# Performance work log

Hardware: AMD Instinct MI355X
Metric: run time of the kernel (lower is better)

The kernel has to match this reference:

```python
import jax, jax.numpy as jnp
import numpy as np

NUM_ENT = 30000
NUM_ATTR_VALUES = 10000
NUM_NODES = NUM_ENT + NUM_ATTR_VALUES
NUM_REL = 230
NUM_ATTR_TYPES = 10
HIDDEN = 200          # num_bases=200 -> 1x1 block decomposition (per-rel diagonal)
N_EDGES = 600000
TIME_INTERVAL = 24
NUM_TIMESTAMPS = 365
PERIOD = 7
TRANX = 0.1
AMPY = 0.005
BATCH = 4096
RRELU_SLOPE = (1.0 / 8.0 + 1.0 / 3.0) / 2.0  # F.rrelu in eval mode


def setup_inputs() -> dict:
    key = jax.random.key(0)
    ks = jax.random.split(key, 12)
    ent_emb = jax.random.normal(ks[0], (NUM_ENT, HIDDEN), jnp.float32)            # nn.init.normal_
    attr_emb = jax.random.normal(ks[1], (NUM_ATTR_VALUES, HIDDEN), jnp.float32) * 0.05
    rel_emb = jax.random.normal(ks[2], (NUM_REL, HIDDEN), jnp.float32) * 0.1
    t = jnp.arange(NUM_TIMESTAMPS, dtype=jnp.float32)
    time_emb = (AMPY * (jnp.sin(2.0 * jnp.pi * t / PERIOD) + 1.0) + TRANX)[:, None]  # (T,1), frozen
    # RGCNBlockLayer weight: (num_rels, num_bases*submat_in*submat_out) = (10, 200)
    rgcn_weight = jax.random.normal(ks[3], (NUM_ATTR_TYPES, HIDDEN), jnp.float32) * 0.1
    dec_W = jax.random.normal(ks[4], (HIDDEN, 2 * HIDDEN + 1), jnp.float32) * 0.05
    dec_b = jnp.zeros((HIDDEN,), jnp.float32)
    edge_src = jax.random.randint(ks[5], (N_EDGES,), 0, NUM_NODES)
    edge_dst = jax.random.randint(ks[6], (N_EDGES,), 0, NUM_NODES)
    edge_type = jax.random.randint(ks[7], (N_EDGES,), 0, NUM_ATTR_TYPES)
    deg = jax.ops.segment_sum(jnp.ones((N_EDGES,), jnp.float32), edge_dst, num_segments=NUM_NODES)
    norm = (1.0 / jnp.clip(deg, 1.0))[:, None]  # (NUM_NODES, 1) in-degree norm
    ent_idx = jax.random.randint(ks[8], (BATCH,), 0, NUM_ENT)
    rel_idx = jax.random.randint(ks[9], (BATCH,), 0, NUM_REL)
    obj_idx = jax.random.randint(ks[10], (BATCH,), 0, NUM_ENT)
    time_raw = jax.random.randint(ks[11], (BATCH,), 0, NUM_TIMESTAMPS * TIME_INTERVAL)
    batch_data = jnp.stack([ent_idx, rel_idx, obj_idx, time_raw], axis=1)  # (B, 4)
    return {
        'ent_emb': ent_emb, 'attr_emb': attr_emb, 'rel_emb': rel_emb,
        'time_emb': time_emb, 'rgcn_weight': rgcn_weight,
        'dec_W': dec_W, 'dec_b': dec_b, 'norm': norm,
        'edge_src': edge_src, 'edge_dst': edge_dst, 'edge_type': edge_type,
        'batch_data': batch_data,
    }


def reference(ent_emb, attr_emb, rel_emb, time_emb, rgcn_weight, dec_W, dec_b,
              norm, edge_src, edge_dst, edge_type, batch_data):
    # --- RGCNBlockLayer (1x1 blocks): gather, per-relation diagonal multiply, scatter-sum ---
    h0 = jnp.concatenate([ent_emb, attr_emb], axis=0)           # (N, H)
    msg = h0[edge_src] * rgcn_weight[edge_type]                  # (E, H)
    agg = jax.ops.segment_sum(msg, edge_dst, num_segments=h0.shape[0])
    h = agg * norm                                               # apply_func: h * norm
    h = jnp.where(h >= 0, h, RRELU_SLOPE * h)                    # rrelu (eval); dropout=identity
    static_emb = h[:NUM_ENT]                                     # (num_ent, H)
    # --- embedding lookups ---
    ent = static_emb[batch_data[:, 0]]                           # (B, H)
    rel = rel_emb[batch_data[:, 1]]                              # (B, H)
    tim = time_emb[batch_data[:, 3] // TIME_INTERVAL]            # (B, 1)
    # --- decoder: tanh -> cat -> linear -> (dropout) -> relu -> mm ---
    x = jnp.concatenate([jnp.tanh(ent), rel, tim], axis=1)       # (B, 2H+1)
    x = x @ dec_W.T + dec_b                                      # (B, H)
    x = jax.nn.relu(x)
    return x @ static_emb.T                                      # (B, num_ent)
```

## Files before the change

### kernel.cpp

```cpp
#include <hip/hip_runtime.h>
#include <hip/hip_bf16.h>

#define NUM_ENT   30000
#define NUM_ATTR  10000
#define NUM_NODES 40000
#define NUM_TYPES 10
#define HIDDEN    200
#define KPAD      224
#define XP        416
#define NPAD      30080
#define N_EDGES   600000
#define BATCH     4096
#define XDIM      401
#define RRELU_SLOPE 0.22916666666666666f

using bf16x8 = __attribute__((ext_vector_type(8))) short;
using f32x4  = __attribute__((ext_vector_type(4))) float;
typedef __hip_bfloat16 bf16;

__device__ inline float bf2f(ushort u) { return __uint_as_float((unsigned)u << 16); }

__global__ void k_cvt(const float* __restrict__ ent, const float* __restrict__ attr,
                      ushort* __restrict__ h0b) {
    int i4 = blockIdx.x * blockDim.x + threadIdx.x;
    if (i4 >= NUM_NODES * HIDDEN / 4) return;
    int base = i4 * 4;
    const float* src = (base < NUM_ENT * HIDDEN) ? ent + base
                                                 : attr + (base - NUM_ENT * HIDDEN);
    float4 v = *reinterpret_cast<const float4*>(src);
    ushort4 o;
    o.x = __bfloat16_as_ushort(__float2bfloat16(v.x));
    o.y = __bfloat16_as_ushort(__float2bfloat16(v.y));
    o.z = __bfloat16_as_ushort(__float2bfloat16(v.z));
    o.w = __bfloat16_as_ushort(__float2bfloat16(v.w));
    *reinterpret_cast<ushort4*>(h0b + base) = o;
}

__global__ __launch_bounds__(1024) void k_prep(const float* __restrict__ norm,
                                               int* __restrict__ offsets,
                                               int* __restrict__ cursor) {
    __shared__ int part[1024];
    int t = threadIdx.x;
    const int CH = (NUM_ENT + 1023) / 1024;
    int base = t * CH;
    int caps[CH];
    int s = 0;
    for (int i = 0; i < CH; ++i) {
        int idx = base + i;
        int c = 0;
        if (idx < NUM_ENT) c = (int)(1.0f / norm[idx] + 0.5f);
        caps[i] = c;
        s += c;
    }
    part[t] = s;
    __syncthreads();
    for (int off = 1; off < 1024; off <<= 1) {
        int v = (t >= off) ? part[t - off] : 0;
        __syncthreads();
        part[t] += v;
        __syncthreads();
    }
    int run = (t == 0) ? 0 : part[t - 1];
    for (int i = 0; i < CH; ++i) {
        int idx = base + i;
        if (idx < NUM_ENT) {
            offsets[idx] = run;
            cursor[idx]  = run;
            run += caps[i];
        }
    }
}

__global__ void k_place(const int* __restrict__ edst, const int* __restrict__ esrc,
                        const int* __restrict__ etype, int* __restrict__ cursor,
                        int* __restrict__ sorted) {
    int e = blockIdx.x * blockDim.x + threadIdx.x;
    if (e < N_EDGES) {
        int d = edst[e];
        if (d < NUM_ENT) {
            int p = atomicAdd(&cursor[d], 1);
            sorted[p] = (esrc[e] << 4) | etype[e];
        }
    }
}

__global__ void k_aggregate(const ushort* __restrict__ h0b, const float* __restrict__ w,
                            const int* __restrict__ offsets, const int* __restrict__ cursor,
                            const int* __restrict__ sorted, const float* __restrict__ norm,
                            bf16* __restrict__ S) {
    __shared__ float wl[NUM_TYPES * HIDDEN];
    for (int i = threadIdx.x; i < NUM_TYPES * HIDDEN; i += blockDim.x)
        wl[i] = w[i];
    __syncthreads();

    int n    = (blockIdx.x * blockDim.x + threadIdx.x) >> 6;
    int lane = threadIdx.x & 63;
    if (n >= NPAD) return;

    if (n >= NUM_ENT) {
        if (lane < KPAD / 4) {
            bf16 z4[4] = {};
            *reinterpret_cast<uint2*>(S + (size_t)n * KPAD + lane * 4) =
                *reinterpret_cast<uint2*>(z4);
        }
        return;
    }

    int beg = offsets[n], end = cursor[n];
    bool act = lane < 50;
    int  c   = lane * 4;

    float4 a0 = make_float4(0, 0, 0, 0), a1 = a0, a2 = a0, a3 = a0;
    int e = beg;
    for (; e + 4 <= end; e += 4) {
        int r0 = sorted[e + 0], r1 = sorted[e + 1], r2 = sorted[e + 2], r3 = sorted[e + 3];
        if (act) {
            ushort4 h0 = *reinterpret_cast<const ushort4*>(h0b + (size_t)(r0 >> 4) * HIDDEN + c);
            ushort4 h1 = *reinterpret_cast<const ushort4*>(h0b + (size_t)(r1 >> 4) * HIDDEN + c);
            ushort4 h2 = *reinterpret_cast<const ushort4*>(h0b + (size_t)(r2 >> 4) * HIDDEN + c);
            ushort4 h3 = *reinterpret_cast<const ushort4*>(h0b + (size_t)(r3 >> 4) * HIDDEN + c);
            const float* w0 = &wl[(r0 & 15) * HIDDEN + c];
            const float* w1 = &wl[(r1 & 15) * HIDDEN + c];
            const float* w2 = &wl[(r2 & 15) * HIDDEN + c];
            const float* w3 = &wl[(r3 & 15) * HIDDEN + c];
            a0.x += bf2f(h0.x) * w0[0]; a0.y += bf2f(h0.y) * w0[1];
            a0.z += bf2f(h0.z) * w0[2]; a0.w += bf2f(h0.w) * w0[3];
            a1.x += bf2f(h1.x) * w1[0]; a1.y += bf2f(h1.y) * w1[1];
            a1.z += bf2f(h1.z) * w1[2]; a1.w += bf2f(h1.w) * w1[3];
            a2.x += bf2f(h2.x) * w2[0]; a2.y += bf2f(h2.y) * w2[1];
            a2.z += bf2f(h2.z) * w2[2]; a2.w += bf2f(h2.w) * w2[3];
            a3.x += bf2f(h3.x) * w3[0]; a3.y += bf2f(h3.y) * w3[1];
            a3.z += bf2f(h3.z) * w3[2]; a3.w += bf2f(h3.w) * w3[3];
        }
    }
    for (; e < end; ++e) {
        int r0 = sorted[e];
        if (act) {
            ushort4 h0 = *reinterpret_cast<const ushort4*>(h0b + (size_t)(r0 >> 4) * HIDDEN + c);
            const float* w0 = &wl[(r0 & 15) * HIDDEN + c];
            a0.x += bf2f(h0.x) * w0[0]; a0.y += bf2f(h0.y) * w0[1];
            a0.z += bf2f(h0.z) * w0[2]; a0.w += bf2f(h0.w) * w0[3];
        }
    }

    if (act) {
        float nm = norm[n];
        float v0 = (a0.x + a1.x + a2.x + a3.x) * nm;
        float v1 = (a0.y + a1.y + a2.y + a3.y) * nm;
        float v2 = (a0.z + a1.z + a2.z + a3.z) * nm;
        float v3 = (a0.w + a1.w + a2.w + a3.w) * nm;
        v0 = (v0 >= 0.f) ? v0 : RRELU_SLOPE * v0;
        v1 = (v1 >= 0.f) ? v1 : RRELU_SLOPE * v1;
        v2 = (v2 >= 0.f) ? v2 : RRELU_SLOPE * v2;
        v3 = (v3 >= 0.f) ? v3 : RRELU_SLOPE * v3;
        bf16 t4[4] = {__float2bfloat16(v0), __float2bfloat16(v1),
                      __float2bfloat16(v2), __float2bfloat16(v3)};
        *reinterpret_cast<uint2*>(S + (size_t)n * KPAD + lane * 4) =
            *reinterpret_cast<uint2*>(t4);
    } else if (lane < KPAD / 4) {
        bf16 z4[4] = {};
        *reinterpret_cast<uint2*>(S + (size_t)n * KPAD + lane * 4) =
            *reinterpret_cast<uint2*>(z4);
    }
}

__global__ void k_build_XW(const bf16* __restrict__ S, const float* __restrict__ rel_emb,
                           const float* __restrict__ time_emb, const float* __restrict__ dec_W,
                           const int* __restrict__ batch, bf16* __restrict__ X,
                           bf16* __restrict__ Wb) {
    int b = blockIdx.x;
    if (b < BATCH) {
        int m = b;
        int e  = batch[m * 4 + 0];
        int rl = batch[m * 4 + 1];
        int tr = batch[m * 4 + 3];
        float tv = time_emb[tr / 24];
        for (int c = threadIdx.x; c < XP; c += 256) {
            float v;
            if (c < HIDDEN) {
                v = tanhf(__bfloat162float(S[(size_t)e * KPAD + c]));
            } else if (c < 2 * HIDDEN) {
                v = rel_emb[(size_t)rl * HIDDEN + (c - HIDDEN)];
            } else if (c == 2 * HIDDEN) {
                v = tv;
            } else {
                v = 0.f;
            }
            X[(size_t)m * XP + c] = __float2bfloat16(v);
        }
    } else {
        int n = b - BATCH;
        for (int c = threadIdx.x; c < XP; c += 256) {
            float v = (n < HIDDEN && c < XDIM) ? dec_W[(size_t)n * XDIM + c] : 0.f;
            Wb[(size_t)n * XP + c] = __float2bfloat16(v);
        }
    }
}

__global__ __launch_bounds__(256) void k_dec_gemm(const bf16* __restrict__ Xb,
                                                  const bf16* __restrict__ Wbb,
                                                  const float* __restrict__ dec_b,
                                                  bf16* __restrict__ Y) {
    int wid  = threadIdx.x >> 6;
    int lane = threadIdx.x & 63;
    int row0 = blockIdx.x * 64 + wid * 16;
    int rsel = lane & 15;
    int koff = (lane >> 4) * 8;

    const short* Xp = reinterpret_cast<const short*>(Xb);
    const short* Wp = reinterpret_cast<const short*>(Wbb);

    f32x4 acc[14] = {};
#pragma unroll
    for (int kt = 0; kt < 13; ++kt) {
        int kbase = kt * 32 + koff;
        bf16x8 a = *reinterpret_cast<const bf16x8*>(Xp + (size_t)(row0 + rsel) * XP + kbase);
#pragma unroll
        for (int j = 0; j < 14; ++j) {
            bf16x8 b = *reinterpret_cast<const bf16x8*>(Wp + (size_t)(j * 16 + rsel) * XP + kbase);
            acc[j] = __builtin_amdgcn_mfma_f32_16x16x32_bf16(a, b, acc[j], 0, 0, 0);
        }
    }

    int crow = (lane >> 4) * 4;
    int ccol = lane & 15;
#pragma unroll
    for (int j = 0; j < 14; ++j) {
        int col = j * 16 + ccol;
        float bias = (col < HIDDEN) ? dec_b[col] : 0.f;
#pragma unroll
        for (int r = 0; r < 4; ++r) {
            int row = row0 + crow + r;
            float v = fmaxf(acc[j][r] + bias, 0.f);
            Y[(size_t)row * KPAD + col] = __float2bfloat16(v);
        }
    }
}

__global__ __launch_bounds__(256) void k_gemm(const bf16* __restrict__ Yb,
                                              const bf16* __restrict__ Sb,
                                              float* __restrict__ out) {
    int bid = blockIdx.x;
    int xcd = bid & 7;
    int t   = (bid >> 3) + xcd * 940;
    int ytile = t & 31;
    int xtile = t >> 5;

    int wid  = threadIdx.x >> 6;
    int lane = threadIdx.x & 63;
    int wm = wid >> 1, wn = wid & 1;
    int row0 = ytile * 128 + wm * 64;
    int col0 = xtile * 128 + wn * 64;
    int rsel = lane & 15;
    int koff = (lane >> 4) * 8;

    const short* Yp = reinterpret_cast<const short*>(Yb);
    const short* Sp = reinterpret_cast<const short*>(Sb);

    f32x4 acc[4][4] = {};
#pragma unroll
    for (int kt = 0; kt < 7; ++kt) {
        int kbase = kt * 32 + koff;
        bf16x8 a[4], b[4];
#pragma unroll
        for (int i = 0; i < 4; ++i)
            a[i] = *reinterpret_cast<const bf16x8*>(Yp + (size_t)(row0 + i * 16 + rsel) * KPAD + kbase);
#pragma unroll
        for (int j = 0; j < 4; ++j)
            b[j] = *reinterpret_cast<const bf16x8*>(Sp + (size_t)(col0 + j * 16 + rsel) * KPAD + kbase);
#pragma unroll
        for (int i = 0; i < 4; ++i)
#pragma unroll
            for (int j = 0; j < 4; ++j)
                acc[i][j] = __builtin_amdgcn_mfma_f32_16x16x32_bf16(a[i], b[j], acc[i][j], 0, 0, 0);
    }

    int crow = (lane >> 4) * 4;
    int ccol = lane & 15;
#pragma unroll
    for (int i = 0; i < 4; ++i)
#pragma unroll
        for (int j = 0; j < 4; ++j) {
            int col = col0 + j * 16 + ccol;
            if (col >= NUM_ENT) continue;
#pragma unroll
            for (int r = 0; r < 4; ++r) {
                int row = row0 + i * 16 + crow + r;
                out[(size_t)row * NUM_ENT + col] = acc[i][j][r];
            }
        }
}

extern "C" void kernel_launch(void* const* d_in, const int* in_sizes, int n_in,
                              void* d_out, int out_size, void* d_ws, size_t ws_size,
                              hipStream_t stream) {
    const float* ent_emb  = (const float*)d_in[0];
    const float* attr_emb = (const float*)d_in[1];
    const float* rel_emb  = (const float*)d_in[2];
    const float* time_emb = (const float*)d_in[3];
    const float* rgcn_w   = (const float*)d_in[4];
    const float* dec_W    = (const float*)d_in[5];
    const float* dec_b    = (const float*)d_in[6];
    const float* norm     = (const float*)d_in[7];
    const int*   esrc     = (const int*)d_in[8];
    const int*   edst     = (const int*)d_in[9];
    const int*   etype    = (const int*)d_in[10];
    const int*   batch    = (const int*)d_in[11];

    char* ws = (char*)d_ws;
    bf16*   S      = (bf16*)ws;
    bf16*   Y      = (bf16*)(ws + 13475840);
    int*    offs   = (int*)(ws + 15310848);
    int*    cursor = (int*)(ws + 15430912);
    int*    sorted = (int*)(ws + 15550976);
    bf16*   X      = (bf16*)(ws + 18070976);
    bf16*   Wb     = (bf16*)(ws + 21478848);
    ushort* h0b    = (ushort*)(ws + 21665216);

    k_cvt  <<<(NUM_NODES * HIDDEN / 4 + 255) / 256, 256, 0, stream>>>(ent_emb, attr_emb, h0b);
    k_prep <<<1, 1024, 0, stream>>>(norm, offs, cursor);
    k_place<<<(N_EDGES + 255) / 256, 256, 0, stream>>>(edst, esrc, etype, cursor, sorted);
    k_aggregate<<<NPAD * 64 / 256, 256, 0, stream>>>(h0b, rgcn_w, offs, cursor, sorted, norm, S);
    k_build_XW<<<BATCH + KPAD, 256, 0, stream>>>(S, rel_emb, time_emb, dec_W, batch, X, Wb);
    k_dec_gemm<<<BATCH / 64, 256, 0, stream>>>(X, Wb, dec_b, Y);
    k_gemm<<<7520, 256, 0, stream>>>(Y, S, (float*)d_out);
}
```

Baseline: 395.2 us.

## Split node aggregation across two waves and stage GEMM output through LDS

```diff
diff --git a/kernel.cpp b/kernel.cpp
--- a/kernel.cpp
+++ b/kernel.cpp
@@ -89,78 +89,93 @@
                             const int* __restrict__ sorted, const float* __restrict__ norm,
                             bf16* __restrict__ S) {
     __shared__ float wl[NUM_TYPES * HIDDEN];
+    __shared__ float part[2][200];
     for (int i = threadIdx.x; i < NUM_TYPES * HIDDEN; i += blockDim.x)
         wl[i] = w[i];
     __syncthreads();
 
-    int n    = (blockIdx.x * blockDim.x + threadIdx.x) >> 6;
+    int wid  = threadIdx.x >> 6;
     int lane = threadIdx.x & 63;
-    if (n >= NPAD) return;
-
-    if (n >= NUM_ENT) {
-        if (lane < KPAD / 4) {
+    int ln   = wid >> 1;
+    int sub  = wid & 1;
+    int n    = blockIdx.x * 2 + ln;
+    bool live = (n < NUM_ENT);
+    bool act  = lane < 50;
+    int  c    = lane * 4;
+
+    float4 a0 = make_float4(0, 0, 0, 0), a1 = a0, a2 = a0, a3 = a0;
+    if (live) {
+        int beg = offsets[n], end = cursor[n];
+        int mid = beg + ((end - beg + 1) >> 1);
+        int lo = sub ? mid : beg;
+        int hi = sub ? end : mid;
+        int e = lo;
+        for (; e + 4 <= hi; e += 4) {
+            int r0 = sorted[e + 0], r1 = sorted[e + 1], r2 = sorted[e + 2], r3 = sorted[e + 3];
+            if (act) {
+                ushort4 h0 = *reinterpret_cast<const ushort4*>(h0b + (size_t)(r0 >> 4) * HIDDEN + c);
+                ushort4 h1 = *reinterpret_cast<const ushort4*>(h0b + (size_t)(r1 >> 4) * HIDDEN + c);
+                ushort4 h2 = *reinterpret_cast<const ushort4*>(h0b + (size_t)(r2 >> 4) * HIDDEN + c);
+                ushort4 h3 = *reinterpret_cast<const ushort4*>(h0b + (size_t)(r3 >> 4) * HIDDEN + c);
+                const float* w0 = &wl[(r0 & 15) * HIDDEN + c];
+                const float* w1 = &wl[(r1 & 15) * HIDDEN + c];
+                const float* w2 = &wl[(r2 & 15) * HIDDEN + c];
+                const float* w3 = &wl[(r3 & 15) * HIDDEN + c];
+                a0.x += bf2f(h0.x) * w0[0]; a0.y += bf2f(h0.y) * w0[1];
+                a0.z += bf2f(h0.z) * w0[2]; a0.w += bf2f(h0.w) * w0[3];
+                a1.x += bf2f(h1.x) * w1[0]; a1.y += bf2f(h1.y) * w1[1];
+                a1.z += bf2f(h1.z) * w1[2]; a1.w += bf2f(h1.w) * w1[3];
+                a2.x += bf2f(h2.x) * w2[0]; a2.y += bf2f(h2.y) * w2[1];
+                a2.z += bf2f(h2.z) * w2[2]; a2.w += bf2f(h2.w) * w2[3];
+                a3.x += bf2f(h3.x) * w3[0]; a3.y += bf2f(h3.y) * w3[1];
+                a3.z += bf2f(h3.z) * w3[2]; a3.w += bf2f(h3.w) * w3[3];
+            }
+        }
+        for (; e < hi; ++e) {
+            int r0 = sorted[e];
+            if (act) {
+                ushort4 h0 = *reinterpret_cast<const ushort4*>(h0b + (size_t)(r0 >> 4) * HIDDEN + c);
+                const float* w0 = &wl[(r0 & 15) * HIDDEN + c];
+                a0.x += bf2f(h0.x) * w0[0]; a0.y += bf2f(h0.y) * w0[1];
+                a0.z += bf2f(h0.z) * w0[2]; a0.w += bf2f(h0.w) * w0[3];
+            }
+        }
+    }
+    float4 acc = make_float4(a0.x + a1.x + a2.x + a3.x,
+                             a0.y + a1.y + a2.y + a3.y,
+                             a0.z + a1.z + a2.z + a3.z,
+                             a0.w + a1.w + a2.w + a3.w);
+    if (live && sub == 1 && act)
+        *reinterpret_cast<float4*>(&part[ln][c]) = acc;
+    __syncthreads();
+
+    if (sub == 0) {
+        if (!live) {
+            if (lane < KPAD / 4) {
+                bf16 z4[4] = {};
+                *reinterpret_cast<uint2*>(S + (size_t)n * KPAD + lane * 4) =
+                    *reinterpret_cast<uint2*>(z4);
+            }
+        } else if (act) {
+            float4 o = *reinterpret_cast<float4*>(&part[ln][c]);
+            float nm = norm[n];
+            float v0 = (acc.x + o.x) * nm;
+            float v1 = (acc.y + o.y) * nm;
+            float v2 = (acc.z + o.z) * nm;
+            float v3 = (acc.w + o.w) * nm;
+            v0 = (v0 >= 0.f) ? v0 : RRELU_SLOPE * v0;
+            v1 = (v1 >= 0.f) ? v1 : RRELU_SLOPE * v1;
+            v2 = (v2 >= 0.f) ? v2 : RRELU_SLOPE * v2;
+            v3 = (v3 >= 0.f) ? v3 : RRELU_SLOPE * v3;
+            bf16 t4[4] = {__float2bfloat16(v0), __float2bfloat16(v1),
+                          __float2bfloat16(v2), __float2bfloat16(v3)};
+            *reinterpret_cast<uint2*>(S + (size_t)n * KPAD + lane * 4) =
+                *reinterpret_cast<uint2*>(t4);
+        } else if (lane < KPAD / 4) {
             bf16 z4[4] = {};
             *reinterpret_cast<uint2*>(S + (size_t)n * KPAD + lane * 4) =
                 *reinterpret_cast<uint2*>(z4);
         }
-        return;
-    }
-
-    int beg = offsets[n], end = cursor[n];
-    bool act = lane < 50;
-    int  c   = lane * 4;
-
-    float4 a0 = make_float4(0, 0, 0, 0), a1 = a0, a2 = a0, a3 = a0;
-    int e = beg;
-    for (; e + 4 <= end; e += 4) {
-        int r0 = sorted[e + 0], r1 = sorted[e + 1], r2 = sorted[e + 2], r3 = sorted[e + 3];
-        if (act) {
-            ushort4 h0 = *reinterpret_cast<const ushort4*>(h0b + (size_t)(r0 >> 4) * HIDDEN + c);
-            ushort4 h1 = *reinterpret_cast<const ushort4*>(h0b + (size_t)(r1 >> 4) * HIDDEN + c);
-            ushort4 h2 = *reinterpret_cast<const ushort4*>(h0b + (size_t)(r2 >> 4) * HIDDEN + c);
-            ushort4 h3 = *reinterpret_cast<const ushort4*>(h0b + (size_t)(r3 >> 4) * HIDDEN + c);
-            const float* w0 = &wl[(r0 & 15) * HIDDEN + c];
-            const float* w1 = &wl[(r1 & 15) * HIDDEN + c];
-            const float* w2 = &wl[(r2 & 15) * HIDDEN + c];
-            const float* w3 = &wl[(r3 & 15) * HIDDEN + c];
-            a0.x += bf2f(h0.x) * w0[0]; a0.y += bf2f(h0.y) * w0[1];
-            a0.z += bf2f(h0.z) * w0[2]; a0.w += bf2f(h0.w) * w0[3];
-            a1.x += bf2f(h1.x) * w1[0]; a1.y += bf2f(h1.y) * w1[1];
-            a1.z += bf2f(h1.z) * w1[2]; a1.w += bf2f(h1.w) * w1[3];
-            a2.x += bf2f(h2.x) * w2[0]; a2.y += bf2f(h2.y) * w2[1];
-            a2.z += bf2f(h2.z) * w2[2]; a2.w += bf2f(h2.w) * w2[3];
-            a3.x += bf2f(h3.x) * w3[0]; a3.y += bf2f(h3.y) * w3[1];
-            a3.z += bf2f(h3.z) * w3[2]; a3.w += bf2f(h3.w) * w3[3];
-        }
-    }
-    for (; e < end; ++e) {
-        int r0 = sorted[e];
-        if (act) {
-            ushort4 h0 = *reinterpret_cast<const ushort4*>(h0b + (size_t)(r0 >> 4) * HIDDEN + c);
-            const float* w0 = &wl[(r0 & 15) * HIDDEN + c];
-            a0.x += bf2f(h0.x) * w0[0]; a0.y += bf2f(h0.y) * w0[1];
-            a0.z += bf2f(h0.z) * w0[2]; a0.w += bf2f(h0.w) * w0[3];
-        }
-    }
-
-    if (act) {
-        float nm = norm[n];
-        float v0 = (a0.x + a1.x + a2.x + a3.x) * nm;
-        float v1 = (a0.y + a1.y + a2.y + a3.y) * nm;
-        float v2 = (a0.z + a1.z + a2.z + a3.z) * nm;
-        float v3 = (a0.w + a1.w + a2.w + a3.w) * nm;
-        v0 = (v0 >= 0.f) ? v0 : RRELU_SLOPE * v0;
-        v1 = (v1 >= 0.f) ? v1 : RRELU_SLOPE * v1;
-        v2 = (v2 >= 0.f) ? v2 : RRELU_SLOPE * v2;
-        v3 = (v3 >= 0.f) ? v3 : RRELU_SLOPE * v3;
-        bf16 t4[4] = {__float2bfloat16(v0), __float2bfloat16(v1),
-                      __float2bfloat16(v2), __float2bfloat16(v3)};
-        *reinterpret_cast<uint2*>(S + (size_t)n * KPAD + lane * 4) =
-            *reinterpret_cast<uint2*>(t4);
-    } else if (lane < KPAD / 4) {
-        bf16 z4[4] = {};
-        *reinterpret_cast<uint2*>(S + (size_t)n * KPAD + lane * 4) =
-            *reinterpret_cast<uint2*>(z4);
     }
 }
 
@@ -240,6 +255,8 @@
 __global__ __launch_bounds__(256) void k_gemm(const bf16* __restrict__ Yb,
                                               const bf16* __restrict__ Sb,
                                               float* __restrict__ out) {
+    __shared__ float eb[4][32 * 68];
+
     int bid = blockIdx.x;
     int xcd = bid & 7;
     int t   = (bid >> 3) + xcd * 940;
@@ -275,20 +292,31 @@
                 acc[i][j] = __builtin_amdgcn_mfma_f32_16x16x32_bf16(a[i], b[j], acc[i][j], 0, 0, 0);
     }
 
-    int crow = (lane >> 4) * 4;
-    int ccol = lane & 15;
-#pragma unroll
-    for (int i = 0; i < 4; ++i)
-#pragma unroll
-        for (int j = 0; j < 4; ++j) {
-            int col = col0 + j * 16 + ccol;
-            if (col >= NUM_ENT) continue;
-#pragma unroll
-            for (int r = 0; r < 4; ++r) {
-                int row = row0 + i * 16 + crow + r;
-                out[(size_t)row * NUM_ENT + col] = acc[i][j][r];
-            }
-        }
+    float* myeb = eb[wid];
+    int hi16 = lane >> 4;
+    int lo16 = lane & 15;
+#pragma unroll
+    for (int h = 0; h < 2; ++h) {
+        if (h) __syncthreads();
+#pragma unroll
+        for (int ii = 0; ii < 2; ++ii)
+#pragma unroll
+            for (int j = 0; j < 4; ++j)
+#pragma unroll
+                for (int r = 0; r < 4; ++r)
+                    myeb[(ii * 16 + hi16 * 4 + r) * 68 + j * 16 + lo16] = acc[h * 2 + ii][j][r];
+        __syncthreads();
+#pragma unroll
+        for (int q = 0; q < 8; ++q) {
+            int lr = q * 4 + hi16;
+            int lc = lo16 * 4;
+            float4 v = *reinterpret_cast<float4*>(&myeb[lr * 68 + lc]);
+            int grow = row0 + h * 32 + lr;
+            int gcol = col0 + lc;
+            if (gcol < NUM_ENT)
+                *reinterpret_cast<float4*>(&out[(size_t)grow * NUM_ENT + gcol]) = v;
+        }
+    }
 }
 
 extern "C" void kernel_launch(void* const* d_in, const int* in_sizes, int n_in,
@@ -320,7 +348,7 @@
     k_cvt  <<<(NUM_NODES * HIDDEN / 4 + 255) / 256, 256, 0, stream>>>(ent_emb, attr_emb, h0b);
     k_prep <<<1, 1024, 0, stream>>>(norm, offs, cursor);
     k_place<<<(N_EDGES + 255) / 256, 256, 0, stream>>>(edst, esrc, etype, cursor, sorted);
-    k_aggregate<<<NPAD * 64 / 256, 256, 0, stream>>>(h0b, rgcn_w, offs, cursor, sorted, norm, S);
+    k_aggregate<<<NPAD / 2, 256, 0, stream>>>(h0b, rgcn_w, offs, cursor, sorted, norm, S);
     k_build_XW<<<BATCH + KPAD, 256, 0, stream>>>(S, rel_emb, time_emb, dec_W, batch, X, Wb);
     k_dec_gemm<<<BATCH / 64, 256, 0, stream>>>(X, Wb, dec_b, Y);
     k_gemm<<<7520, 256, 0, stream>>>(Y, S, (float*)d_out);
```

After: 400.8 us. Within noise of the previous version (+1.4%).
